# Optimization experiments

Hardware: AMD Instinct MI355X
Metric: run time of the kernel (lower is better)

Reference implementation:

```python
import jax, jax.numpy as jnp
import numpy as np

B, T, D, L, E = 8, 2048, 256, 8, 64


def setup_inputs() -> dict:
    key = jax.random.key(0)
    ks = jax.random.split(key, 5)
    x = jax.random.normal(ks[0], (B, T, D), dtype=jnp.float32)
    # MMLP params: weight (4L, D, E), bias (4L, E); nn.Linear: (2L, D), (2L,)
    W_ml = jax.random.normal(ks[1], (4 * L, D, E), dtype=jnp.float32) * 0.05
    b_ml = jax.random.normal(ks[2], (4 * L, E), dtype=jnp.float32) * 0.05
    W_lin = jax.random.normal(ks[3], (2 * L, D), dtype=jnp.float32) * 0.05
    b_lin = jax.random.normal(ks[4], (2 * L,), dtype=jnp.float32) * 0.05
    return {"x": x, "W_ml": W_ml, "b_ml": b_ml, "W_lin": W_lin, "b_lin": b_lin}


def _xlstm_forward(x, W_ml, b_ml, W_lin, b_lin):
    b, t, _ = x.shape
    l4, _, e = W_ml.shape
    l = l4 // 4
    # Precompute all per-step gate projections at once (the torch code does this per step).
    mg = jnp.einsum('bti,lij->btlj', x, W_ml) + b_ml          # (B,T,4L,E)
    lg = jnp.einsum('bti,li->btl', x, W_lin) + b_lin          # (B,T,2L)
    o_, v, k, q = jnp.split(mg, 4, axis=2)                    # each (B,T,L,E)
    i_, f_ = jnp.split(lg, 2, axis=2)                         # each (B,T,L)
    xs = tuple(jnp.moveaxis(a, 1, 0) for a in (o_, v, k, q, i_, f_))  # time-major

    def step(carry, inp):
        m, n, C, h = carry
        o_t, v_t, k_t, q_t, i_t, f_t = inp
        m_new = jnp.maximum(f_t + m, i_t)                     # stabilizer (B,L)
        i_g = jnp.exp(i_t - m_new)
        f_g = jnp.exp(f_t + m - m_new)
        # rank-1 outer-product update of matrix cell state (B,L,E,E)
        C = f_g[:, :, None, None] * C + i_g[:, :, None, None] * (v_t[:, :, :, None] * k_t[:, :, None, :])
        n = f_g[:, :, None] * n + i_g[:, :, None] * k_t       # (B,L,E)
        denom = jnp.maximum(jnp.sum(n * q_t, axis=-1), 1.0)[:, :, None]  # clamp(.,1,inf)
        h = jax.nn.sigmoid(o_t) * jnp.einsum('blij,bli->blj', C, q_t) / denom
        return (m_new, n, C, h), None

    init = (
        jnp.zeros((b, l), jnp.float32),
        jnp.zeros((b, l, e), jnp.float32),
        jnp.zeros((b, l, e, e), jnp.float32),
        jnp.zeros((b, l, e), jnp.float32),
    )
    (m, n, C, h), _ = jax.lax.scan(step, init, xs)
    return h, C


def reference(x, W_ml, b_ml, W_lin, b_lin):
    return _xlstm_forward(x, W_ml, b_ml, W_lin, b_lin)
```

## Files before the change

### kernel.cpp

```cpp
#include <hip/hip_runtime.h>

#define B 8
#define T 2048
#define D 256
#define L 8
#define E 64
#define BT (B*T)

typedef _Float16 f16;
typedef f16 f16x8 __attribute__((ext_vector_type(8)));
typedef float f32x4 __attribute__((ext_vector_type(4)));

#define OFF_I   0
#define OFF_F   (OFF_I  + B*L*T)
#define OFF_W16 (OFF_F  + B*L*T)
#define OFF_WT  (OFF_W16 + B*L*T/2)
#define OFF_VT  (OFF_WT + 16*E*D/2)
#define OFF_KT  (OFF_VT + B*L*E*T/2)
#define OFF_CP  (OFF_KT + B*L*E*T/2)

__global__ __launch_bounds__(256) void k_prep(const float* __restrict__ x,
        const float* __restrict__ Wlin, const float* __restrict__ blin,
        const float* __restrict__ Wml,
        float* __restrict__ ibuf, float* __restrict__ fbuf,
        f16* __restrict__ Wt16) {
    __shared__ __align__(16) char smem[49920];
    int tid = threadIdx.x;
    int bx = blockIdx.x;
    if (bx < 512) {
        float (*xs)[260] = (float(*)[260])smem;
        float (*wsm)[260] = (float(*)[260])(smem + 33280);
        int t0 = bx * 32;
        {
            int row = tid >> 3, q = tid & 7;
            const float* src = x + (size_t)(t0 + row) * D + q * 32;
            #pragma unroll
            for (int j = 0; j < 8; ++j) {
                float4 v = *(const float4*)(src + j * 4);
                *(float4*)&xs[row][q * 32 + j * 4] = v;
            }
        }
        {
            int row = tid >> 4, c0 = (tid & 15) * 16;
            const float* src = Wlin + row * D + c0;
            #pragma unroll
            for (int j = 0; j < 4; ++j) {
                float4 v = *(const float4*)(src + j * 4);
                *(float4*)&wsm[row][c0 + j * 4] = v;
            }
        }
        __syncthreads();
        int tl = tid >> 4, g = tid & 15;
        float acc0 = 0.f, acc1 = 0.f;
        for (int i = 0; i < D; ++i) {
            float wv = wsm[g][i];
            acc0 += xs[tl * 2 + 0][i] * wv;
            acc1 += xs[tl * 2 + 1][i] * wv;
        }
        float bias = blin[g];
        float acc[2] = {acc0 + bias, acc1 + bias};
        #pragma unroll
        for (int u = 0; u < 2; ++u) {
            int t = t0 + tl * 2 + u;
            int b = t >> 11, tt = t & 2047;
            if (g < 8) ibuf[(b * L + g) * T + tt] = acc[u];
            else       fbuf[(b * L + (g - 8)) * T + tt] = acc[u];
        }
    } else {
        float (*ts)[65] = (float(*)[65])smem;
        int vkrow = bx - 512;
        int wrow = 8 + vkrow;
        for (int dc = 0; dc < 4; ++dc) {
            int d0 = dc * 64;
            int r = tid >> 2, cq = (tid & 3) * 16;
            const float* src = Wml + ((size_t)wrow * D + d0 + r) * E + cq;
            #pragma unroll
            for (int j = 0; j < 16; j += 4) {
                float4 v = *(const float4*)(src + j);
                ts[r][cq + j] = v.x; ts[r][cq + j + 1] = v.y;
                ts[r][cq + j + 2] = v.z; ts[r][cq + j + 3] = v.w;
            }
            __syncthreads();
            int e = tid >> 2, dq = (tid & 3) * 16;
            f16* dst = Wt16 + ((size_t)vkrow * E + e) * D + d0 + dq;
            f16x8 o0, o1;
            #pragma unroll
            for (int j = 0; j < 8; ++j) {
                o0[j] = (f16)ts[dq + j][e];
                o1[j] = (f16)ts[dq + 8 + j][e];
            }
            *(f16x8*)dst = o0;
            *(f16x8*)(dst + 8) = o1;
            __syncthreads();
        }
    }
}

__global__ __launch_bounds__(256) void k_scan(const float* __restrict__ ibuf,
        const float* __restrict__ fbuf, f16* __restrict__ w16) {
    __shared__ float part[256];
    __shared__ float red[256];
    int tid = threadIdx.x;
    int base = blockIdx.x * T;
    const float* fp = fbuf + base + tid * 8;
    const float* ip = ibuf + base + tid * 8;
    float4 fa = *(const float4*)fp;
    float4 fb = *(const float4*)(fp + 4);
    float4 ia = *(const float4*)ip;
    float4 ib = *(const float4*)(ip + 4);
    float f[8] = {fa.x, fa.y, fa.z, fa.w, fb.x, fb.y, fb.z, fb.w};
    float iv[8] = {ia.x, ia.y, ia.z, ia.w, ib.x, ib.y, ib.z, ib.w};
    float ls[8]; float run = 0.f;
    #pragma unroll
    for (int r = 0; r < 8; ++r) { run += f[r]; ls[r] = run; }
    part[tid] = run;
    __syncthreads();
    if (tid == 0) {
        float running = 0.f;
        for (int k = 0; k < 256; ++k) { float tmp = part[k]; part[k] = running; running += tmp; }
    }
    __syncthreads();
    float off = part[tid];
    float e[8]; float lmax = -1e30f;
    #pragma unroll
    for (int r = 0; r < 8; ++r) { e[r] = iv[r] - (off + ls[r]); lmax = fmaxf(lmax, e[r]); }
    red[tid] = lmax;
    __syncthreads();
    for (int s = 128; s > 0; s >>= 1) {
        if (tid < s) red[tid] = fmaxf(red[tid], red[tid + s]);
        __syncthreads();
    }
    float M = fmaxf(red[0], 0.0f);
    f16x8 wv8;
    #pragma unroll
    for (int r = 0; r < 8; ++r) wv8[r] = (f16)__expf(e[r] - M);
    *(f16x8*)(w16 + base + tid * 8) = wv8;
}

__global__ __launch_bounds__(256) void k_vkproj2(const float* __restrict__ x,
        const f16* __restrict__ Wt16, const float* __restrict__ bml,
        f16* __restrict__ Vt, f16* __restrict__ Kt) {
    __shared__ __align__(16) char lds[32768];
    int tid = threadIdx.x;
    int bx = blockIdx.x, l = blockIdx.y;
    int t0 = bx * 128;
    const float* xa = x + (size_t)t0 * D;
    const f16* wvp = Wt16 + (size_t)l * E * D;
    const f16* wkp = Wt16 + (size_t)(8 + l) * E * D;
    int wv = tid >> 6, lane = tid & 63;
    f32x4 acc[2][8] = {};
    for (int kc = 0; kc < 4; ++kc) {
        int k0 = kc * 64;
        #pragma unroll
        for (int q = 0; q < 4; ++q) {
            int idx = q * 256 + tid;
            int row = idx >> 3, c = idx & 7;
            const float* src = xa + (size_t)row * D + k0 + c * 8;
            float4 v0 = *(const float4*)src;
            float4 v1 = *(const float4*)(src + 4);
            f16x8 h;
            h[0] = (f16)v0.x; h[1] = (f16)v0.y; h[2] = (f16)v0.z; h[3] = (f16)v0.w;
            h[4] = (f16)v1.x; h[5] = (f16)v1.y; h[6] = (f16)v1.z; h[7] = (f16)v1.w;
            int ba = (row * 128 + c * 16) ^ ((row & 7) << 4);
            *(f16x8*)(lds + ba) = h;
        }
        #pragma unroll
        for (int q = 0; q < 4; ++q) {
            int idx = q * 256 + tid;
            int row = idx >> 3, c = idx & 7;
            const f16* src = (row < 64 ? wvp + (size_t)row * D
                                       : wkp + (size_t)(row - 64) * D) + k0 + c * 8;
            f16x8 v = *(const f16x8*)src;
            int ba = 16384 + ((row * 128 + c * 16) ^ ((row & 7) << 4));
            *(f16x8*)(lds + ba) = v;
        }
        __syncthreads();
        #pragma unroll
        for (int kk = 0; kk < 2; ++kk) {
            int ko = kk * 32 + (lane >> 4) * 8;
            f16x8 a[2], bf[8];
            #pragma unroll
            for (int fr = 0; fr < 2; ++fr) {
                int row = wv * 32 + fr * 16 + (lane & 15);
                int ba = (row * 128 + ko * 2) ^ ((row & 7) << 4);
                a[fr] = *(const f16x8*)(lds + ba);
            }
            #pragma unroll
            for (int fc = 0; fc < 8; ++fc) {
                int e = fc * 16 + (lane & 15);
                int ba = 16384 + ((e * 128 + ko * 2) ^ ((e & 7) << 4));
                bf[fc] = *(const f16x8*)(lds + ba);
            }
            #pragma unroll
            for (int fr = 0; fr < 2; ++fr)
                #pragma unroll
                for (int fc = 0; fc < 8; ++fc)
                    acc[fr][fc] = __builtin_amdgcn_mfma_f32_16x16x32_f16(
                        a[fr], bf[fc], acc[fr][fc], 0, 0, 0);
        }
        __syncthreads();
    }
    const float* bvp = bml + (size_t)(8 + l) * E;
    const float* bkp = bml + (size_t)(16 + l) * E;
    #pragma unroll
    for (int fc = 0; fc < 8; ++fc) {
        int e = fc * 16 + (lane & 15);
        float bias = (e < 64) ? bvp[e] : bkp[e - 64];
        int swz = (e & 7) << 4;
        #pragma unroll
        for (int fr = 0; fr < 2; ++fr) {
            #pragma unroll
            for (int r = 0; r < 4; r += 2) {
                int t = wv * 32 + fr * 16 + (lane >> 4) * 4 + r;
                union { f16 h[2]; unsigned u; } pk;
                pk.h[0] = (f16)(acc[fr][fc][r] + bias);
                pk.h[1] = (f16)(acc[fr][fc][r + 1] + bias);
                int ba = (e * 256 + t * 2) ^ swz;
                *(unsigned*)(lds + ba) = pk.u;
            }
        }
    }
    __syncthreads();
    int e2 = tid >> 1, tq = (tid & 1) * 64;
    int bb = t0 >> 11, tin = t0 & 2047;
    int vk = e2 >> 6, el = e2 & 63;
    f16* dst = (vk ? Kt : Vt) + ((size_t)((bb * L + l) * E + el)) * T + tin + tq;
    int swz = (e2 & 7) << 4;
    #pragma unroll
    for (int j = 0; j < 8; ++j) {
        int ba = (e2 * 256 + (tq + j * 8) * 2) ^ swz;
        *(f16x8*)(dst + j * 8) = *(const f16x8*)(lds + ba);
    }
}

__global__ __launch_bounds__(256) void k_cgemm2(const f16* __restrict__ Vt,
        const f16* __restrict__ Kt, const f16* __restrict__ w16,
        float* __restrict__ Cpart) {
    __shared__ float red[64 * 64];
    __shared__ float redn[64];
    int tid = threadIdx.x;
    int bl = blockIdx.x, tc = blockIdx.y;
    int wv = tid >> 6, lane = tid & 63;
    const f16* vp = Vt + (size_t)bl * E * T;
    const f16* kp = Kt + (size_t)bl * E * T;
    const f16* wp = w16 + (size_t)bl * T;
    f32x4 acc[5][4] = {};
    int tbase = tc * 512 + wv * 128;
    for (int kc = 0; kc < 4; ++kc) {
        int tt = tbase + kc * 32 + (lane >> 4) * 8;
        f16x8 wfrag = *(const f16x8*)(wp + tt);
        f16x8 a[5], bf[4];
        #pragma unroll
        for (int m = 0; m < 4; ++m) {
            int i = m * 16 + (lane & 15);
            f16x8 v = *(const f16x8*)(vp + (size_t)i * T + tt);
            a[m] = v * wfrag;
        }
        a[4] = wfrag;
        #pragma unroll
        for (int nn = 0; nn < 4; ++nn) {
            int j = nn * 16 + (lane & 15);
            bf[nn] = *(const f16x8*)(kp + (size_t)j * T + tt);
        }
        #pragma unroll
        for (int m = 0; m < 5; ++m)
            #pragma unroll
            for (int nn = 0; nn < 4; ++nn)
                acc[m][nn] = __builtin_amdgcn_mfma_f32_16x16x32_f16(
                    a[m], bf[nn], acc[m][nn], 0, 0, 0);
    }
    for (int rr = 0; rr < 4; ++rr) {
        if (wv == rr) {
            #pragma unroll
            for (int m = 0; m < 4; ++m)
                #pragma unroll
                for (int nn = 0; nn < 4; ++nn)
                    #pragma unroll
                    for (int r = 0; r < 4; ++r) {
                        int row = m * 16 + (lane >> 4) * 4 + r;
                        int col = nn * 16 + (lane & 15);
                        if (rr == 0) red[row * 64 + col] = acc[m][nn][r];
                        else         red[row * 64 + col] += acc[m][nn][r];
                    }
            if ((lane >> 4) == 0) {
                #pragma unroll
                for (int nn = 0; nn < 4; ++nn) {
                    int col = nn * 16 + (lane & 15);
                    if (rr == 0) redn[col] = acc[4][nn][0];
                    else         redn[col] += acc[4][nn][0];
                }
            }
        }
        __syncthreads();
    }
    float* cp = Cpart + ((size_t)bl * 4 + tc) * 4160;
    #pragma unroll
    for (int j = 0; j < 4; ++j) {
        int idx = tid * 16 + j * 4;
        *(float4*)(cp + idx) = *(const float4*)(red + idx);
    }
    if (tid < 64) cp[4096 + tid] = redn[tid];
}

__global__ __launch_bounds__(256) void k_final(const float* __restrict__ x,
        const float* __restrict__ Wml, const float* __restrict__ bml,
        const float* __restrict__ Cpart, float* __restrict__ out) {
    __shared__ float Cs[E * E];
    __shared__ float xs[D];
    __shared__ float ns[E];
    __shared__ float os[E];
    __shared__ float qs[E];
    int tid = threadIdx.x;
    int bl = blockIdx.x; int b = bl >> 3, l = bl & 7;
    xs[tid] = x[((size_t)(b * T + (T - 1))) * D + tid];
    const float* cp = Cpart + (size_t)bl * 4 * 4160;
    #pragma unroll
    for (int j = 0; j < 4; ++j) {
        int idx = tid * 16 + j * 4;
        float4 s = {0, 0, 0, 0};
        #pragma unroll
        for (int p = 0; p < 4; ++p) {
            float4 v = *(const float4*)(cp + p * 4160 + idx);
            s.x += v.x; s.y += v.y; s.z += v.z; s.w += v.w;
        }
        *(float4*)&Cs[idx] = s;
        *(float4*)(out + 4096 + (size_t)bl * (E * E) + idx) = s;
    }
    if (tid < 64) {
        float s = 0.f;
        #pragma unroll
        for (int p = 0; p < 4; ++p) s += cp[p * 4160 + 4096 + tid];
        ns[tid] = s;
    }
    __syncthreads();
    if (tid < 128) {
        int gate = tid >> 6, e = tid & 63;
        int wrow = gate ? (3 * L + l) : l;
        const float* wpp = Wml + (size_t)wrow * D * E + e;
        float s = 0.f;
        for (int kk = 0; kk < D; ++kk) s += xs[kk] * wpp[kk * E];
        s += bml[wrow * E + e];
        if (gate) qs[e] = s; else os[e] = s;
    }
    __syncthreads();
    if (tid < 64) {
        int j = tid;
        float hc = 0.f;
        for (int i2 = 0; i2 < E; ++i2) hc += Cs[i2 * E + j] * qs[i2];
        float nq = 0.f;
        for (int i2 = 0; i2 < E; ++i2) nq += ns[i2] * qs[i2];
        float denom = fmaxf(nq, 1.0f);
        float sg = 1.0f / (1.0f + __expf(-os[j]));
        out[bl * E + j] = sg * hc / denom;
    }
}

extern "C" void kernel_launch(void* const* d_in, const int* in_sizes, int n_in,
                              void* d_out, int out_size, void* d_ws, size_t ws_size,
                              hipStream_t stream) {
    const float* x    = (const float*)d_in[0];
    const float* Wml  = (const float*)d_in[1];
    const float* bml  = (const float*)d_in[2];
    const float* Wlin = (const float*)d_in[3];
    const float* blin = (const float*)d_in[4];
    float* out = (float*)d_out;
    float* ws = (float*)d_ws;
    float* ibuf  = ws + OFF_I;
    float* fbuf  = ws + OFF_F;
    f16*   w16   = (f16*)(ws + OFF_W16);
    f16*   Wt16  = (f16*)(ws + OFF_WT);
    f16*   Vt    = (f16*)(ws + OFF_VT);
    f16*   Kt    = (f16*)(ws + OFF_KT);
    float* Cpart = ws + OFF_CP;

    k_prep<<<512 + 16, 256, 0, stream>>>(x, Wlin, blin, Wml, ibuf, fbuf, Wt16);
    k_scan<<<B * L, 256, 0, stream>>>(ibuf, fbuf, w16);
    k_vkproj2<<<dim3(BT / 128, 8), 256, 0, stream>>>(x, Wt16, bml, Vt, Kt);
    k_cgemm2<<<dim3(B * L, 4), 256, 0, stream>>>(Vt, Kt, w16, Cpart);
    k_final<<<B * L, 256, 0, stream>>>(x, Wml, bml, Cpart, out);
}
```

Before: 75.46 us.

## Pre-convert x to fp16 and widen V/K projection tiles across all heads

Adds a kernel that converts x to fp16 once. The V/K projection is restructured so each 512-thread block computes a 128x512 tile covering all 8 heads of V or of K, instead of one head at a time. This means x is read once per block rather than 8 times, and the fp32-to-fp16 conversion is not redone for every head. The serial single-thread prefix sum in k_scan is replaced by a parallel Hillis-Steele scan. The trade-off is an extra launch, an extra round trip of x16 through global memory, and higher register pressure from the 4x8 accumulator tile.

```diff
diff --git a/kernel.cpp b/kernel.cpp
--- a/kernel.cpp
+++ b/kernel.cpp
@@ -18,6 +18,18 @@
 #define OFF_VT  (OFF_WT + 16*E*D/2)
 #define OFF_KT  (OFF_VT + B*L*E*T/2)
 #define OFF_CP  (OFF_KT + B*L*E*T/2)
+#define OFF_X16 (OFF_CP + 64*4*4160)
+
+__global__ __launch_bounds__(256) void k_prep_x(const float* __restrict__ x,
+                                                f16* __restrict__ x16) {
+    int i = (blockIdx.x * 256 + threadIdx.x) * 8;
+    float4 v0 = *(const float4*)(x + i);
+    float4 v1 = *(const float4*)(x + i + 4);
+    f16x8 o;
+    o[0] = (f16)v0.x; o[1] = (f16)v0.y; o[2] = (f16)v0.z; o[3] = (f16)v0.w;
+    o[4] = (f16)v1.x; o[5] = (f16)v1.y; o[6] = (f16)v1.z; o[7] = (f16)v1.w;
+    *(f16x8*)(x16 + i) = o;
+}
 
 __global__ __launch_bounds__(256) void k_prep(const float* __restrict__ x,
         const float* __restrict__ Wlin, const float* __restrict__ blin,
@@ -115,12 +127,16 @@
     for (int r = 0; r < 8; ++r) { run += f[r]; ls[r] = run; }
     part[tid] = run;
     __syncthreads();
-    if (tid == 0) {
-        float running = 0.f;
-        for (int k = 0; k < 256; ++k) { float tmp = part[k]; part[k] = running; running += tmp; }
-    }
-    __syncthreads();
-    float off = part[tid];
+    float inc = run;
+    #pragma unroll
+    for (int s = 1; s < 256; s <<= 1) {
+        float u = (tid >= s) ? part[tid - s] : 0.f;
+        __syncthreads();
+        inc += u;
+        part[tid] = inc;
+        __syncthreads();
+    }
+    float off = inc - run;
     float e[8]; float lmax = -1e30f;
     #pragma unroll
     for (int r = 0; r < 8; ++r) { e[r] = iv[r] - (off + ls[r]); lmax = fmaxf(lmax, e[r]); }
@@ -137,99 +153,96 @@
     *(f16x8*)(w16 + base + tid * 8) = wv8;
 }
 
-__global__ __launch_bounds__(256) void k_vkproj2(const float* __restrict__ x,
+__global__ __launch_bounds__(512) void k_vkproj3(const f16* __restrict__ x16,
         const f16* __restrict__ Wt16, const float* __restrict__ bml,
         f16* __restrict__ Vt, f16* __restrict__ Kt) {
-    __shared__ __align__(16) char lds[32768];
-    int tid = threadIdx.x;
-    int bx = blockIdx.x, l = blockIdx.y;
+    __shared__ __align__(16) char lds[40960];
+    int tid = threadIdx.x;
+    int bx = blockIdx.x, h = blockIdx.y;
     int t0 = bx * 128;
-    const float* xa = x + (size_t)t0 * D;
-    const f16* wvp = Wt16 + (size_t)l * E * D;
-    const f16* wkp = Wt16 + (size_t)(8 + l) * E * D;
+    const f16* xa = x16 + (size_t)t0 * D;
+    const f16* wb = Wt16 + (size_t)h * 8 * E * D;
     int wv = tid >> 6, lane = tid & 63;
-    f32x4 acc[2][8] = {};
-    for (int kc = 0; kc < 4; ++kc) {
-        int k0 = kc * 64;
-        #pragma unroll
-        for (int q = 0; q < 4; ++q) {
-            int idx = q * 256 + tid;
-            int row = idx >> 3, c = idx & 7;
-            const float* src = xa + (size_t)row * D + k0 + c * 8;
-            float4 v0 = *(const float4*)src;
-            float4 v1 = *(const float4*)(src + 4);
-            f16x8 h;
-            h[0] = (f16)v0.x; h[1] = (f16)v0.y; h[2] = (f16)v0.z; h[3] = (f16)v0.w;
-            h[4] = (f16)v1.x; h[5] = (f16)v1.y; h[6] = (f16)v1.z; h[7] = (f16)v1.w;
-            int ba = (row * 128 + c * 16) ^ ((row & 7) << 4);
-            *(f16x8*)(lds + ba) = h;
-        }
-        #pragma unroll
-        for (int q = 0; q < 4; ++q) {
-            int idx = q * 256 + tid;
-            int row = idx >> 3, c = idx & 7;
-            const f16* src = (row < 64 ? wvp + (size_t)row * D
-                                       : wkp + (size_t)(row - 64) * D) + k0 + c * 8;
-            f16x8 v = *(const f16x8*)src;
-            int ba = 16384 + ((row * 128 + c * 16) ^ ((row & 7) << 4));
+    int wr = wv >> 2, wc = wv & 3;
+    int q = lane >> 4, lr = lane & 15;
+    int sa_t = tid >> 2, sa_q = tid & 3;
+    f32x4 acc[4][8] = {};
+    for (int ks = 0; ks < 8; ++ks) {
+        int k0 = ks * 32;
+        {
+            f16x8 v = *(const f16x8*)(xa + (size_t)sa_t * D + k0 + sa_q * 8);
+            int ba = sa_t * 64 + ((sa_q ^ ((sa_t >> 1) & 3)) << 4);
             *(f16x8*)(lds + ba) = v;
         }
-        __syncthreads();
-        #pragma unroll
-        for (int kk = 0; kk < 2; ++kk) {
-            int ko = kk * 32 + (lane >> 4) * 8;
-            f16x8 a[2], bf[8];
-            #pragma unroll
-            for (int fr = 0; fr < 2; ++fr) {
-                int row = wv * 32 + fr * 16 + (lane & 15);
-                int ba = (row * 128 + ko * 2) ^ ((row & 7) << 4);
-                a[fr] = *(const f16x8*)(lds + ba);
-            }
-            #pragma unroll
-            for (int fc = 0; fc < 8; ++fc) {
-                int e = fc * 16 + (lane & 15);
-                int ba = 16384 + ((e * 128 + ko * 2) ^ ((e & 7) << 4));
-                bf[fc] = *(const f16x8*)(lds + ba);
-            }
-            #pragma unroll
-            for (int fr = 0; fr < 2; ++fr)
+        #pragma unroll
+        for (int rr = 0; rr < 4; ++rr) {
+            int r = rr * 128 + (tid >> 2);
+            int c = tid & 3;
+            f16x8 v = *(const f16x8*)(wb + (size_t)r * D + k0 + c * 8);
+            int ba = 8192 + r * 64 + ((c ^ ((r >> 1) & 3)) << 4);
+            *(f16x8*)(lds + ba) = v;
+        }
+        __syncthreads();
+        f16x8 a[4], bf[8];
+        #pragma unroll
+        for (int m = 0; m < 4; ++m) {
+            int t = wr * 64 + m * 16 + lr;
+            int ba = t * 64 + ((q ^ ((t >> 1) & 3)) << 4);
+            a[m] = *(const f16x8*)(lds + ba);
+        }
+        #pragma unroll
+        for (int n = 0; n < 8; ++n) {
+            int c = wc * 128 + n * 16 + lr;
+            int ba = 8192 + c * 64 + ((q ^ ((c >> 1) & 3)) << 4);
+            bf[n] = *(const f16x8*)(lds + ba);
+        }
+        #pragma unroll
+        for (int m = 0; m < 4; ++m)
+            #pragma unroll
+            for (int n = 0; n < 8; ++n)
+                acc[m][n] = __builtin_amdgcn_mfma_f32_16x16x32_f16(
+                    a[m], bf[n], acc[m][n], 0, 0, 0);
+        __syncthreads();
+    }
+    const float* bp = bml + (size_t)(8 + h * 8) * E;
+    int b_g = t0 >> 11, tin = t0 & 2047;
+    f16* obase = h ? Kt : Vt;
+    for (int p = 0; p < 4; ++p) {
+        if (wc == p) {
+            #pragma unroll
+            for (int n = 0; n < 8; ++n) {
+                int cc = n * 16 + lr;
+                float bias = bp[p * 128 + cc];
+                int swz = (cc & 7) << 4;
                 #pragma unroll
-                for (int fc = 0; fc < 8; ++fc)
-                    acc[fr][fc] = __builtin_amdgcn_mfma_f32_16x16x32_f16(
-                        a[fr], bf[fc], acc[fr][fc], 0, 0, 0);
-        }
-        __syncthreads();
-    }
-    const float* bvp = bml + (size_t)(8 + l) * E;
-    const float* bkp = bml + (size_t)(16 + l) * E;
-    #pragma unroll
-    for (int fc = 0; fc < 8; ++fc) {
-        int e = fc * 16 + (lane & 15);
-        float bias = (e < 64) ? bvp[e] : bkp[e - 64];
-        int swz = (e & 7) << 4;
-        #pragma unroll
-        for (int fr = 0; fr < 2; ++fr) {
-            #pragma unroll
-            for (int r = 0; r < 4; r += 2) {
-                int t = wv * 32 + fr * 16 + (lane >> 4) * 4 + r;
-                union { f16 h[2]; unsigned u; } pk;
-                pk.h[0] = (f16)(acc[fr][fc][r] + bias);
-                pk.h[1] = (f16)(acc[fr][fc][r + 1] + bias);
-                int ba = (e * 256 + t * 2) ^ swz;
-                *(unsigned*)(lds + ba) = pk.u;
-            }
-        }
-    }
-    __syncthreads();
-    int e2 = tid >> 1, tq = (tid & 1) * 64;
-    int bb = t0 >> 11, tin = t0 & 2047;
-    int vk = e2 >> 6, el = e2 & 63;
-    f16* dst = (vk ? Kt : Vt) + ((size_t)((bb * L + l) * E + el)) * T + tin + tq;
-    int swz = (e2 & 7) << 4;
-    #pragma unroll
-    for (int j = 0; j < 8; ++j) {
-        int ba = (e2 * 256 + (tq + j * 8) * 2) ^ swz;
-        *(f16x8*)(dst + j * 8) = *(const f16x8*)(lds + ba);
+                for (int m = 0; m < 4; ++m) {
+                    #pragma unroll
+                    for (int r = 0; r < 4; r += 2) {
+                        int t = wr * 64 + m * 16 + q * 4 + r;
+                        union { f16 h2[2]; unsigned u; } pk;
+                        pk.h2[0] = (f16)(acc[m][n][r] + bias);
+                        pk.h2[1] = (f16)(acc[m][n][r + 1] + bias);
+                        int ba = cc * 256 + ((t * 2) ^ swz);
+                        *(unsigned*)(lds + ba) = pk.u;
+                    }
+                }
+            }
+        }
+        __syncthreads();
+        {
+            int cc = tid >> 2, part = tid & 3;
+            int cg = p * 128 + cc;
+            int l = cg >> 6, e = cg & 63;
+            f16* dst = obase + ((size_t)((b_g * L + l) * E + e)) * T + tin + part * 32;
+            int swz = (cc & 7) << 4;
+            #pragma unroll
+            for (int jj = 0; jj < 4; ++jj) {
+                int t = part * 32 + jj * 8;
+                int ba = cc * 256 + ((t * 2) ^ swz);
+                *(f16x8*)(dst + jj * 8) = *(const f16x8*)(lds + ba);
+            }
+        }
+        __syncthreads();
     }
 }
 
@@ -372,10 +385,12 @@
     f16*   Vt    = (f16*)(ws + OFF_VT);
     f16*   Kt    = (f16*)(ws + OFF_KT);
     float* Cpart = ws + OFF_CP;
-
+    f16*   x16   = (f16*)(ws + OFF_X16);
+
+    k_prep_x<<<BT * D / (256 * 8), 256, 0, stream>>>(x, x16);
     k_prep<<<512 + 16, 256, 0, stream>>>(x, Wlin, blin, Wml, ibuf, fbuf, Wt16);
     k_scan<<<B * L, 256, 0, stream>>>(ibuf, fbuf, w16);
-    k_vkproj2<<<dim3(BT / 128, 8), 256, 0, stream>>>(x, Wt16, bml, Vt, Kt);
+    k_vkproj3<<<dim3(BT / 128, 2), 512, 0, stream>>>(x16, Wt16, bml, Vt, Kt);
     k_cgemm2<<<dim3(B * L, 4), 256, 0, stream>>>(Vt, Kt, w16, Cpart);
     k_final<<<B * L, 256, 0, stream>>>(x, Wml, bml, Cpart, out);
 }
```

Measured after the change: 71.39 us. 1.06x faster.
